# Kernel tuning notes

Measured on AMD Instinct MI355X. Metric: run time of the kernel, lower is better.

Reference implementation:

```python
import jax, jax.numpy as jnp
import numpy as np

N_NODES = 30000
N_EDGES = 480000
IN_SIZE = 256
EDGE_FEAT = 32
N_TOWERS = 4
DELTA = 2.5


def setup_inputs():
    key = jax.random.key(0)
    ks = jax.random.split(key, 8)
    T, d = N_TOWERS, IN_SIZE // N_TOWERS
    m_in = 2 * d + EDGE_FEAT                 # M: Linear(2*tower_in+edge_feat -> tower_in)
    u_in = (4 * 3 + 1) * d                   # U: Linear((n_agg*n_scaler+1)*tower_in -> tower_out)
    return {
        "n_feat": jax.random.normal(ks[0], (N_NODES, IN_SIZE), jnp.float32),
        "e_feat": jax.random.normal(ks[1], (N_EDGES, EDGE_FEAT), jnp.float32),
        "src": jax.random.randint(ks[2], (N_EDGES,), 0, N_NODES),
        "dst": jax.random.randint(ks[3], (N_EDGES,), 0, N_NODES),
        "M_w": jax.random.normal(ks[4], (T, d, m_in), jnp.float32) * (1.0 / np.sqrt(m_in)),
        "M_b": jnp.zeros((T, d), jnp.float32),
        "U_w": jax.random.normal(ks[5], (T, d, u_in), jnp.float32) * (1.0 / np.sqrt(u_in)),
        "U_b": jnp.zeros((T, d), jnp.float32),
        "bn_gamma": jnp.ones((T, d), jnp.float32),
        "bn_beta": jnp.zeros((T, d), jnp.float32),
        "mix_w": jax.random.normal(ks[6], (IN_SIZE, IN_SIZE), jnp.float32) * (1.0 / np.sqrt(IN_SIZE)),
        "mix_b": jnp.zeros((IN_SIZE,), jnp.float32),
    }


def reference(n_feat, e_feat, src, dst, M_w, M_b, U_w, U_b, bn_gamma, bn_beta, mix_w, mix_b):
    N, F = n_feat.shape
    T, d, _ = M_w.shape
    E = src.shape[0]
    h = n_feat.reshape(N, T, d)                                   # towers split the feature dim
    ef = jnp.broadcast_to(e_feat[:, None, :], (E, T, e_feat.shape[1]))
    f = jnp.concatenate([h[src], h[dst], ef], axis=-1)            # [E,T,2d+ef]
    msg = jnp.einsum('eti,toi->eto', f, M_w) + M_b                # per-edge message, [E,T,d]

    deg = jax.ops.segment_sum(jnp.ones((E,), msg.dtype), dst, num_segments=N)  # in-degree
    degc = jnp.maximum(deg, 1.0)[:, None, None]
    s = jax.ops.segment_sum(msg, dst, num_segments=N)
    ssq = jax.ops.segment_sum(msg * msg, dst, num_segments=N)
    mean = s / degc
    var = jax.nn.relu(ssq / degc - mean * mean)                   # DGL aggregate_var
    std = jnp.sqrt(var + 1e-30)                                   # DGL aggregate_std
    has = (deg > 0.0)[:, None, None]
    mx = jnp.where(has, jax.ops.segment_max(msg, dst, num_segments=N), 0.0)
    mn = jnp.where(has, jax.ops.segment_min(msg, dst, num_segments=N), 0.0)
    agg = jnp.concatenate([mean, mx, mn, std], axis=-1)           # [N,T,4d]

    logd = jnp.log(deg + 1.0)
    amp = (logd / DELTA)[:, None, None]                            # amplification scaler
    att = jnp.where(deg > 0.0, DELTA / jnp.maximum(logd, 1e-12), 0.0)[:, None, None]  # attenuation
    hsc = jnp.concatenate([agg, agg * amp, agg * att], axis=-1)   # [N,T,12d]

    u_in = jnp.concatenate([h, hsc], axis=-1)                     # [N,T,13d]
    u = jnp.einsum('nti,toi->nto', u_in, U_w) + U_b               # [N,T,d]
    mu = jnp.mean(u, axis=0)
    v = jnp.mean((u - mu) ** 2, axis=0)
    u = (u - mu) / jnp.sqrt(v + 1e-5) * bn_gamma + bn_beta        # BatchNorm1d (training mode)

    h_cat = u.reshape(N, F)
    mixed = h_cat @ mix_w.T + mix_b
    mixed = jnp.where(mixed > 0, mixed, 0.01 * mixed)             # LeakyReLU mixing layer
    out = mixed + n_feat                                          # residual (in_size==out_size)
    return jax.nn.relu(out)                                       # last == 0 -> ReLU
```

## Files before the change

### kernel.cpp

```cpp
#include <hip/hip_runtime.h>
#include <math.h>

constexpr float DELTA_ = 2.5f;
#define BN_BLOCKS 512

typedef __attribute__((ext_vector_type(8))) short bf16x8;
typedef __attribute__((ext_vector_type(4))) float f32x4;
typedef __attribute__((ext_vector_type(2))) _Float16 half2_t;

#if defined(__has_builtin)
#if __has_builtin(__builtin_amdgcn_fdot2)
#define DOT2(a,b,c) __builtin_amdgcn_fdot2((a),(b),(c),false)
#endif
#endif
#ifndef DOT2
#define DOT2(a,b,c) fmaf((float)(a).x,(float)(b).x, fmaf((float)(a).y,(float)(b).y,(c)))
#endif

__device__ inline ushort bf16h(float x){
  union { float f; unsigned u; } v; v.f = x;
  unsigned r = v.u + 0x7fffu + ((v.u >> 16) & 1u);
  return (ushort)(r >> 16);
}
__device__ inline float bf16f(ushort h){
  union { unsigned u; float f; } v; v.u = ((unsigned)h) << 16;
  return v.f;
}

__global__ __launch_bounds__(256) void k_tU(const float* __restrict__ Uw, ushort* __restrict__ Wpk2){
  int i = blockIdx.x*256 + threadIdx.x;
  if (i >= 4*192*320) return;
  int k   = i % 320;
  int col = (i/320) % 192;
  int t   = i/(320*192);
  int path = col >> 6, o = col & 63;
  float v = 0.f;
  int src = -1;
  if (k < 64){ if (path == 0) src = k; }
  else        src = k + path*256;
  if (src >= 0) v = Uw[((size_t)(t*64 + o))*832 + src];
  Wpk2[i] = bf16h(v);
}

__global__ __launch_bounds__(256) void k_tMm(const float* __restrict__ mixw, ushort* __restrict__ Wm2){
  int i = blockIdx.x*256 + threadIdx.x;
  if (i >= 256*256) return;
  Wm2[i] = bf16h(mixw[i]);
}

__global__ __launch_bounds__(256) void k_tE(const float* __restrict__ Mw, _Float16* __restrict__ Mwefh){
  int i = blockIdx.x*256 + threadIdx.x;
  if (i >= 256*32) return;
  int k = i & 31, c = i >> 5;
  Mwefh[i] = (_Float16)Mw[(size_t)c*160 + 128 + k];
}

__global__ __launch_bounds__(256) void k_xh(const float* __restrict__ nf, ushort* __restrict__ X2, int N){
  for (long i = blockIdx.x*256 + threadIdx.x; i < (long)N*256; i += (long)gridDim.x*256){
    int n = (int)(i >> 8), c = (int)(i & 255);
    int t = c >> 6, d = c & 63;
    int j = d >> 3, pos = d & 7;
    float v = nf[i];
    ushort hi = bf16h(v);
    size_t base = (((size_t)n*4 + t)*40 + j)*16;
    X2[base + pos]     = hi;
    X2[base + 8 + pos] = bf16h(v - bf16f(hi));
  }
}

__global__ __launch_bounds__(256) void k_hist(const int* __restrict__ dstv, int* __restrict__ cnt, int E){
  int e = blockIdx.x*256 + threadIdx.x;
  if (e < E) atomicAdd(&cnt[dstv[e]], 1);
}

__global__ __launch_bounds__(256) void k_scan1(const int* __restrict__ cnt, int* __restrict__ offs,
                                               int* __restrict__ bsum, int N){
  __shared__ int lds[256];
  int i = threadIdx.x;
  int g = blockIdx.x*256 + i;
  int v = (g < N) ? cnt[g] : 0;
  int acc = v;
  lds[i] = acc; __syncthreads();
  for (int s = 1; s < 256; s <<= 1){
    int t = (i >= s) ? lds[i - s] : 0;
    __syncthreads();
    acc += t; lds[i] = acc;
    __syncthreads();
  }
  if (g < N) offs[g] = acc - v;
  if (i == 255) bsum[blockIdx.x] = acc;
}

__global__ __launch_bounds__(256) void k_scan2(int* __restrict__ bsum, int NB){
  __shared__ int lds[256];
  int i = threadIdx.x;
  int v = (i < NB) ? bsum[i] : 0;
  int acc = v;
  lds[i] = acc; __syncthreads();
  for (int s = 1; s < 256; s <<= 1){
    int t = (i >= s) ? lds[i - s] : 0;
    __syncthreads();
    acc += t; lds[i] = acc;
    __syncthreads();
  }
  if (i < NB) bsum[i] = acc - v;
}

__global__ __launch_bounds__(256) void k_scan3(int* __restrict__ offs, const int* __restrict__ bsum, int N, int E){
  int g = blockIdx.x*256 + threadIdx.x;
  if (g < N) offs[g] += bsum[blockIdx.x];
  if (g == 0) offs[N] = E;
}

__global__ __launch_bounds__(256) void k_fill(const int* __restrict__ dstv, const int* __restrict__ offs,
                                              int* __restrict__ cur, int* __restrict__ elist, int E){
  int e = blockIdx.x*256 + threadIdx.x;
  if (e < E){
    int d = dstv[e];
    elist[offs[d] + atomicAdd(&cur[d], 1)] = e;
  }
}

__global__ __launch_bounds__(256) void k_perm(const int* __restrict__ elist, const int* __restrict__ srcv,
                                              const float* __restrict__ efeat,
                                              int* __restrict__ esrc, _Float16* __restrict__ efh, int E){
  int g = blockIdx.x*256 + threadIdx.x;
  int pos = g >> 3;
  int q   = g & 7;
  if (pos >= E) return;
  int e = elist[pos];
  if (q == 0) esrc[pos] = srcv[e];
  float4 v = *(const float4*)(efeat + (size_t)e*32 + q*4);
  union { ushort4 u; _Float16 h[4]; } cv;
  cv.h[0] = (_Float16)v.x; cv.h[1] = (_Float16)v.y;
  cv.h[2] = (_Float16)v.z; cv.h[3] = (_Float16)v.w;
  *(ushort4*)(efh + (size_t)pos*32 + q*4) = cv.u;
}

__global__ __launch_bounds__(256) void k_ab(const float* __restrict__ nf, const float* __restrict__ Mw,
                                            const float* __restrict__ Mb,
                                            _Float16* __restrict__ A_h, float* __restrict__ B, int N){
  int c = threadIdx.x;
  int t = __builtin_amdgcn_readfirstlane(threadIdx.x >> 6);
  float ws[64], wd[64];
  const float* row = Mw + (size_t)c*160;
#pragma unroll
  for (int k = 0; k < 64; k += 4){
    float4 a = *(const float4*)(row + k);
    float4 b = *(const float4*)(row + 64 + k);
    ws[k]=a.x; ws[k+1]=a.y; ws[k+2]=a.z; ws[k+3]=a.w;
    wd[k]=b.x; wd[k+1]=b.y; wd[k+2]=b.z; wd[k+3]=b.w;
  }
  float bias = Mb[c];
  for (int n = blockIdx.x; n < N; n += gridDim.x){
    const float* h = nf + (size_t)n*256 + t*64;
    float sa = 0.f, sb = 0.f;
#pragma unroll
    for (int k = 0; k < 64; k += 4){
      float4 h4 = *(const float4*)(h + k);
      sa = fmaf(ws[k], h4.x, sa);  sb = fmaf(wd[k], h4.x, sb);
      sa = fmaf(ws[k+1], h4.y, sa); sb = fmaf(wd[k+1], h4.y, sb);
      sa = fmaf(ws[k+2], h4.z, sa); sb = fmaf(wd[k+2], h4.z, sb);
      sa = fmaf(ws[k+3], h4.w, sa); sb = fmaf(wd[k+3], h4.w, sb);
    }
    A_h[(size_t)n*256 + c] = (_Float16)sa;
    B[(size_t)n*256 + c] = sb + bias;
  }
}

__global__ __launch_bounds__(256) void k_agg(const int* __restrict__ offs, const int* __restrict__ esrc,
                                             const _Float16* __restrict__ efh,
                                             const _Float16* __restrict__ A_h, const float* __restrict__ B,
                                             const _Float16* __restrict__ Mwefh,
                                             ushort* __restrict__ X2, float* __restrict__ sc, int N){
  int c = threadIdx.x;
  union Wu { int4 i[4]; half2_t h[16]; } wr;
  {
    const int4* wp = (const int4*)(Mwefh + (size_t)c*32);
    wr.i[0] = wp[0]; wr.i[1] = wp[1]; wr.i[2] = wp[2]; wr.i[3] = wp[3];
  }

  int n = blockIdx.x;
  if (n >= N) return;
  int o0 = __builtin_amdgcn_readfirstlane(offs[n]);
  int o1 = __builtin_amdgcn_readfirstlane(offs[n+1]);
  int cnt = o1 - o0;
  float b0 = B[(size_t)n*256 + c];
  float s = 0.f, ss = 0.f, mx = -__builtin_huge_valf(), mn = __builtin_huge_valf();

  union Eu { int4 i[4]; half2_t h[16]; };

  int i = 0;
  for (; i + 4 <= cnt; i += 4){
    int p = o0 + i;
    int s0 = __builtin_amdgcn_readfirstlane(esrc[p+0]);
    int s1 = __builtin_amdgcn_readfirstlane(esrc[p+1]);
    int s2 = __builtin_amdgcn_readfirstlane(esrc[p+2]);
    int s3 = __builtin_amdgcn_readfirstlane(esrc[p+3]);
    Eu e0, e1, e2, e3;
    {
      const int4* p0 = (const int4*)(efh + (size_t)(p+0)*32);
      const int4* p1 = (const int4*)(efh + (size_t)(p+1)*32);
      const int4* p2 = (const int4*)(efh + (size_t)(p+2)*32);
      const int4* p3 = (const int4*)(efh + (size_t)(p+3)*32);
#pragma unroll
      for (int q = 0; q < 4; ++q){ e0.i[q]=p0[q]; e1.i[q]=p1[q]; e2.i[q]=p2[q]; e3.i[q]=p3[q]; }
    }
    float a0 = (float)A_h[(size_t)s0*256 + c];
    float a1 = (float)A_h[(size_t)s1*256 + c];
    float a2 = (float)A_h[(size_t)s2*256 + c];
    float a3 = (float)A_h[(size_t)s3*256 + c];
    float m0 = b0 + a0;
    float m1 = b0 + a1;
    float m2 = b0 + a2;
    float m3 = b0 + a3;
#pragma unroll
    for (int q = 0; q < 16; ++q){
      m0 = DOT2(e0.h[q], wr.h[q], m0);
      m1 = DOT2(e1.h[q], wr.h[q], m1);
      m2 = DOT2(e2.h[q], wr.h[q], m2);
      m3 = DOT2(e3.h[q], wr.h[q], m3);
    }
    s += m0; s += m1; s += m2; s += m3;
    ss = fmaf(m0, m0, ss); ss = fmaf(m1, m1, ss);
    ss = fmaf(m2, m2, ss); ss = fmaf(m3, m3, ss);
    mx = fmaxf(mx, fmaxf(fmaxf(m0, m1), fmaxf(m2, m3)));
    mn = fminf(mn, fminf(fminf(m0, m1), fminf(m2, m3)));
  }
  for (; i < cnt; ++i){
    int p = o0 + i;
    int sidx = __builtin_amdgcn_readfirstlane(esrc[p]);
    Eu e0;
    {
      const int4* p0 = (const int4*)(efh + (size_t)p*32);
#pragma unroll
      for (int q = 0; q < 4; ++q) e0.i[q] = p0[q];
    }
    float m = b0 + (float)A_h[(size_t)sidx*256 + c];
#pragma unroll
    for (int q = 0; q < 16; ++q) m = DOT2(e0.h[q], wr.h[q], m);
    s += m;
    ss = fmaf(m, m, ss);
    mx = fmaxf(mx, m);
    mn = fminf(mn, m);
  }

  float deg  = (float)cnt;
  float degc = fmaxf(deg, 1.f);
  float inv  = 1.f / degc;
  float mean = s * inv;
  float var  = fmaxf(ss * inv - mean*mean, 0.f);
  float sd   = sqrtf(var + 1e-30f);
  if (cnt == 0){ mx = 0.f; mn = 0.f; }

  int t = c >> 6, d = c & 63;
#define PUTX(SLOT, VAL) { int kk = 64 + (SLOT)*64 + d; int jj = kk >> 3, pp = kk & 7;      \
    size_t base = (((size_t)n*4 + t)*40 + jj)*16;                                          \
    ushort hi = bf16h(VAL);                                                                \
    X2[base + pp] = hi; X2[base + 8 + pp] = bf16h((VAL) - bf16f(hi)); }
  PUTX(0, mean) PUTX(1, mx) PUTX(2, mn) PUTX(3, sd)
#undef PUTX
  if (c == 0){
    float logd = logf(deg + 1.f);
    sc[(size_t)n*2]     = logd * (1.f / DELTA_);
    sc[(size_t)n*2 + 1] = (cnt > 0) ? (DELTA_ / fmaxf(logd, 1e-12f)) : 0.f;
  }
}

__global__ __launch_bounds__(256) void k_u(const ushort* __restrict__ X2, const ushort* __restrict__ Wpk2,
                                           const float* __restrict__ sc, const float* __restrict__ Ub,
                                           float* __restrict__ uout, int Nn){
  __shared__ float su[64][68];
  int tid = threadIdx.x;
  int t   = blockIdx.y;
  int nbase = blockIdx.x*64;
  int lane = tid & 63, wv = tid >> 6;
  int li = lane & 15, kc = lane >> 4;
  int cbase = wv*48;

  f32x4 acc[4][3];
#pragma unroll
  for (int ri = 0; ri < 4; ++ri)
#pragma unroll
    for (int ci = 0; ci < 3; ++ci) acc[ri][ci] = (f32x4)0.f;

  const ushort* wb = Wpk2 + (size_t)t*192*320;

#pragma unroll 2
  for (int kt = 0; kt < 10; ++kt){
    bf16x8 ah[4], al[4], bh[3];
#pragma unroll
    for (int ri = 0; ri < 4; ++ri){
      int row = nbase + ri*16 + li;
      if (row >= Nn) row = Nn - 1;
      const ushort* ap = X2 + (((size_t)row*4 + t)*40 + kt*4 + kc)*16;
      ah[ri] = *(const bf16x8*)(ap);
      al[ri] = *(const bf16x8*)(ap + 8);
    }
#pragma unroll
    for (int ci = 0; ci < 3; ++ci){
      int col = cbase + ci*16 + li;
      bh[ci] = *(const bf16x8*)(wb + (size_t)col*320 + kt*32 + kc*8);
    }
#pragma unroll
    for (int ci = 0; ci < 3; ++ci)
#pragma unroll
      for (int ri = 0; ri < 4; ++ri){
        acc[ri][ci] = __builtin_amdgcn_mfma_f32_16x16x32_bf16(ah[ri], bh[ci], acc[ri][ci], 0, 0, 0);
        acc[ri][ci] = __builtin_amdgcn_mfma_f32_16x16x32_bf16(al[ri], bh[ci], acc[ri][ci], 0, 0, 0);
      }
  }

#define Y1_STORE(CI, OB) { _Pragma("unroll") for (int ri = 0; ri < 4; ++ri)               \
    { _Pragma("unroll") for (int r = 0; r < 4; ++r)                                        \
      su[ri*16 + kc*4 + r][(OB) + li] = acc[ri][CI][r]; } }
#define Y_ADD(CI, OB, SCOFF) { _Pragma("unroll") for (int ri = 0; ri < 4; ++ri)           \
    { _Pragma("unroll") for (int r = 0; r < 4; ++r){                                       \
      int node = ri*16 + kc*4 + r;                                                        \
      int gn = nbase + node; int gnc = (gn < Nn) ? gn : (Nn - 1);                          \
      float scl = sc[(size_t)gnc*2 + (SCOFF)];                                            \
      su[node][(OB) + li] += scl * acc[ri][CI][r]; } } }

  if (wv == 0){ Y1_STORE(0, 0)  Y1_STORE(1, 16) Y1_STORE(2, 32) }
  else if (wv == 1){ Y1_STORE(0, 48) }
  __syncthreads();
  if (wv == 1){ Y_ADD(1, 0, 0)  Y_ADD(2, 16, 0) }
  else if (wv == 2){ Y_ADD(0, 32, 0) Y_ADD(1, 48, 0) }
  __syncthreads();
  if (wv == 2){ Y_ADD(2, 0, 1) }
  else if (wv == 3){ Y_ADD(0, 16, 1) Y_ADD(1, 32, 1) Y_ADD(2, 48, 1) }
  __syncthreads();
#undef Y1_STORE
#undef Y_ADD

  for (int idx = tid; idx < 64*16; idx += 256){
    int n = idx >> 4, o4 = (idx & 15)*4;
    int gn = nbase + n;
    if (gn < Nn){
      float4 v = *(float4*)(&su[n][o4]);
      const float* ubp = Ub + t*64 + o4;
      v.x += ubp[0]; v.y += ubp[1]; v.z += ubp[2]; v.w += ubp[3];
      *(float4*)(&uout[(size_t)gn*256 + t*64 + o4]) = v;
    }
  }
}

__global__ __launch_bounds__(256) void k_bnstat(const float* __restrict__ u, float* __restrict__ part, int N){
  int c = threadIdx.x;
  int b = blockIdx.x;
  float s = 0.f, ss = 0.f;
  for (int n = b; n < N; n += gridDim.x){
    float v = u[(size_t)n*256 + c];
    s += v;
    ss = fmaf(v, v, ss);
  }
  part[(size_t)b*512 + c]       = s;
  part[(size_t)b*512 + 256 + c] = ss;
}

__global__ __launch_bounds__(256) void k_bnfin(const float* __restrict__ part, const float* __restrict__ gam,
                                               const float* __restrict__ bet, float* __restrict__ bnsc, int N){
  int c = threadIdx.x;
  float s = 0.f, ss = 0.f;
  for (int b = 0; b < BN_BLOCKS; ++b){
    s  += part[(size_t)b*512 + c];
    ss += part[(size_t)b*512 + 256 + c];
  }
  float invN = 1.f / (float)N;
  float mu  = s * invN;
  float ex2 = ss * invN;
  float var = fmaxf(ex2 - mu*mu, 0.f);
  float inv = 1.f / sqrtf(var + 1e-5f);
  float scale = gam[c] * inv;
  bnsc[c]       = scale;
  bnsc[256 + c] = bet[c] - mu*scale;
}

__global__ __launch_bounds__(256) void k_xm(const float* __restrict__ u, const float* __restrict__ bnsc,
                                            ushort* __restrict__ X2m, int N){
  for (long i = blockIdx.x*256 + threadIdx.x; i < (long)N*256; i += (long)gridDim.x*256){
    int n = (int)(i >> 8), c = (int)(i & 255);
    float v = fmaf(u[i], bnsc[c], bnsc[256 + c]);
    int j = c >> 3, pos = c & 7;
    size_t base = ((size_t)n*32 + j)*16;
    ushort hi = bf16h(v);
    X2m[base + pos]     = hi;
    X2m[base + 8 + pos] = bf16h(v - bf16f(hi));
  }
}

__global__ __launch_bounds__(256) void k_mix(const ushort* __restrict__ X2m, const ushort* __restrict__ Wm2,
                                             const float* __restrict__ mixb, const float* __restrict__ nf,
                                             float* __restrict__ outp, int Nn){
  int tid = threadIdx.x;
  int nbase = blockIdx.x*64;
  int lane = tid & 63, wv = tid >> 6;
  int li = lane & 15, kc = lane >> 4;

  f32x4 acc[4][4];
#pragma unroll
  for (int ri = 0; ri < 4; ++ri)
#pragma unroll
    for (int ci = 0; ci < 4; ++ci) acc[ri][ci] = (f32x4)0.f;

#pragma unroll 2
  for (int kt = 0; kt < 8; ++kt){
    bf16x8 ah[4], al[4], bh[4];
#pragma unroll
    for (int ri = 0; ri < 4; ++ri){
      int row = nbase + ri*16 + li;
      if (row >= Nn) row = Nn - 1;
      const ushort* ap = X2m + (((size_t)row*32 + kt*4 + kc))*16;
      ah[ri] = *(const bf16x8*)(ap);
      al[ri] = *(const bf16x8*)(ap + 8);
    }
#pragma unroll
    for (int ci = 0; ci < 4; ++ci){
      int col = wv*64 + ci*16 + li;
      bh[ci] = *(const bf16x8*)(Wm2 + (size_t)col*256 + kt*32 + kc*8);
    }
#pragma unroll
    for (int ci = 0; ci < 4; ++ci)
#pragma unroll
      for (int ri = 0; ri < 4; ++ri){
        acc[ri][ci] = __builtin_amdgcn_mfma_f32_16x16x32_bf16(ah[ri], bh[ci], acc[ri][ci], 0, 0, 0);
        acc[ri][ci] = __builtin_amdgcn_mfma_f32_16x16x32_bf16(al[ri], bh[ci], acc[ri][ci], 0, 0, 0);
      }
  }

#pragma unroll
  for (int ri = 0; ri < 4; ++ri){
#pragma unroll
    for (int r = 0; r < 4; ++r){
      int node = ri*16 + kc*4 + r;
      int gn = nbase + node;
      if (gn < Nn){
#pragma unroll
        for (int ci = 0; ci < 4; ++ci){
          int col = wv*64 + ci*16 + li;
          float m = acc[ri][ci][r] + mixb[col];
          m = (m > 0.f) ? m : 0.01f*m;
          float o = m + nf[(size_t)gn*256 + col];
          outp[(size_t)gn*256 + col] = fmaxf(o, 0.f);
        }
      }
    }
  }
}

extern "C" void kernel_launch(void* const* d_in, const int* in_sizes, int n_in,
                              void* d_out, int out_size, void* d_ws, size_t ws_size,
                              hipStream_t stream){
  const float* nf   = (const float*)d_in[0];
  const float* ef   = (const float*)d_in[1];
  const int*   srcv = (const int*)  d_in[2];
  const int*   dstv = (const int*)  d_in[3];
  const float* Mw   = (const float*)d_in[4];
  const float* Mb   = (const float*)d_in[5];
  const float* Uw   = (const float*)d_in[6];
  const float* Ub   = (const float*)d_in[7];
  const float* gam  = (const float*)d_in[8];
  const float* bet  = (const float*)d_in[9];
  const float* mixw = (const float*)d_in[10];
  const float* mixb = (const float*)d_in[11];
  int N = in_sizes[0] / 256;
  int E = in_sizes[2];
  float* out = (float*)d_out;

  char* wp = (char*)d_ws;
  auto alloc = [&](size_t bytes){
    char* p = wp;
    wp += (bytes + 1023) & ~(size_t)1023;
    return (void*)p;
  };
  int*      cnt   = (int*)     alloc((size_t)N*4);
  int*      offs  = (int*)     alloc((size_t)(N+1)*4);
  int*      cur   = (int*)     alloc((size_t)N*4);
  int*      bsum  = (int*)     alloc(256*4);
  int*      elist = (int*)     alloc((size_t)E*4);
  int*      esrc  = (int*)     alloc((size_t)E*4);
  size_t ealias   = (size_t)E*32*2;
  size_t malias   = (size_t)N*512*2;
  char*     shbuf = (char*)    alloc(ealias > malias ? ealias : malias);
  _Float16* efh   = (_Float16*)shbuf;
  ushort*   X2m   = (ushort*)  shbuf;
  _Float16* A_h   = (_Float16*)alloc((size_t)N*256*2);
  float*    B     = (float*)   alloc((size_t)N*256*4);
  float*    sc    = (float*)   alloc((size_t)N*2*4);
  float*    part  = (float*)   alloc((size_t)BN_BLOCKS*512*4);
  float*    bnsc  = (float*)   alloc(512*4);
  ushort*   X2    = (ushort*)  alloc((size_t)N*4*40*16*2);
  ushort*   Wpk2  = (ushort*)  alloc((size_t)4*192*320*2);
  ushort*   Wm2   = (ushort*)  alloc((size_t)256*256*2);
  _Float16* Mwefh = (_Float16*)alloc((size_t)256*32*2);

  hipMemsetAsync(cnt,  0, (size_t)N*4,  stream);
  hipMemsetAsync(cur,  0, (size_t)N*4,  stream);

  k_tU  <<<(4*192*320 + 255)/256, 256, 0, stream>>>(Uw, Wpk2);
  k_tMm <<<(256*256 + 255)/256, 256, 0, stream>>>(mixw, Wm2);
  k_tE  <<<(256*32 + 255)/256, 256, 0, stream>>>(Mw, Mwefh);
  k_hist<<<(E + 255)/256, 256, 0, stream>>>(dstv, cnt, E);
  k_ab  <<<2048, 256, 0, stream>>>(nf, Mw, Mb, A_h, B, N);
  k_xh  <<<2048, 256, 0, stream>>>(nf, X2, N);

  int NB = (N + 255)/256;
  k_scan1<<<NB, 256, 0, stream>>>(cnt, offs, bsum, N);
  k_scan2<<<1, 256, 0, stream>>>(bsum, NB);
  k_scan3<<<NB, 256, 0, stream>>>(offs, bsum, N, E);
  k_fill <<<(E + 255)/256, 256, 0, stream>>>(dstv, offs, cur, elist, E);
  k_perm <<<(E*8 + 255)/256, 256, 0, stream>>>(elist, srcv, ef, esrc, efh, E);

  k_agg<<<N, 256, 0, stream>>>(offs, esrc, efh, A_h, B, Mwefh, X2, sc, N);

  dim3 ugrid((N + 63)/64, 4);
  k_u<<<ugrid, 256, 0, stream>>>(X2, Wpk2, sc, Ub, out, N);

  k_bnstat<<<BN_BLOCKS, 256, 0, stream>>>(out, part, N);
  k_bnfin <<<1, 256, 0, stream>>>(part, gam, bet, bnsc, N);
  k_xm   <<<2048, 256, 0, stream>>>(out, bnsc, X2m, N);
  k_mix  <<<(N + 63)/64, 256, 0, stream>>>(X2m, Wm2, mixb, nf, out, N);
}
```

Baseline: 493.8 us.

## Compute edge-feature projection with MFMA over edge windows, 8 nodes per block

The aggregation kernel now handles 8 destination nodes per block and walks their contiguous edge range in windows of 64 edges. For each window it computes the edge-feature projection with f16 MFMA instructions into shared memory, replacing per-thread fdot2 loops. It also factors the per-node bias out of the message sums, adding it back algebraically at finalize time. The node-boundary loop is serial and adds syncthreads and a 66KB shared tile, which may reduce occupancy, and the factored variance is numerically less stable.

```diff
diff --git a/kernel.cpp b/kernel.cpp
--- a/kernel.cpp
+++ b/kernel.cpp
@@ -3,19 +3,11 @@
 
 constexpr float DELTA_ = 2.5f;
 #define BN_BLOCKS 512
+#define NPB 8
 
 typedef __attribute__((ext_vector_type(8))) short bf16x8;
+typedef __attribute__((ext_vector_type(8))) _Float16 f16x8;
 typedef __attribute__((ext_vector_type(4))) float f32x4;
-typedef __attribute__((ext_vector_type(2))) _Float16 half2_t;
-
-#if defined(__has_builtin)
-#if __has_builtin(__builtin_amdgcn_fdot2)
-#define DOT2(a,b,c) __builtin_amdgcn_fdot2((a),(b),(c),false)
-#endif
-#endif
-#ifndef DOT2
-#define DOT2(a,b,c) fmaf((float)(a).x,(float)(b).x, fmaf((float)(a).y,(float)(b).y,(c)))
-#endif
 
 __device__ inline ushort bf16h(float x){
   union { float f; unsigned u; } v; v.f = x;
@@ -48,11 +40,15 @@
   Wm2[i] = bf16h(mixw[i]);
 }
 
-__global__ __launch_bounds__(256) void k_tE(const float* __restrict__ Mw, _Float16* __restrict__ Mwefh){
+__global__ __launch_bounds__(256) void k_tE2(const float* __restrict__ Mw, _Float16* __restrict__ Wefp){
   int i = blockIdx.x*256 + threadIdx.x;
-  if (i >= 256*32) return;
-  int k = i & 31, c = i >> 5;
-  Mwefh[i] = (_Float16)Mw[(size_t)c*160 + 128 + k];
+  if (i >= 16*64*8) return;
+  int j    = i & 7;
+  int lane = (i >> 3) & 63;
+  int cb   = i >> 9;
+  int ch = cb*16 + (lane & 15);
+  int k  = ((lane >> 4) & 3)*8 + j;
+  Wefp[i] = (_Float16)Mw[(size_t)ch*160 + 128 + k];
 }
 
 __global__ __launch_bounds__(256) void k_xh(const float* __restrict__ nf, ushort* __restrict__ X2, int N){
@@ -171,100 +167,115 @@
 __global__ __launch_bounds__(256) void k_agg(const int* __restrict__ offs, const int* __restrict__ esrc,
                                              const _Float16* __restrict__ efh,
                                              const _Float16* __restrict__ A_h, const float* __restrict__ B,
-                                             const _Float16* __restrict__ Mwefh,
-                                             ushort* __restrict__ X2, float* __restrict__ sc, int N){
-  int c = threadIdx.x;
-  union Wu { int4 i[4]; half2_t h[16]; } wr;
-  {
-    const int4* wp = (const int4*)(Mwefh + (size_t)c*32);
-    wr.i[0] = wp[0]; wr.i[1] = wp[1]; wr.i[2] = wp[2]; wr.i[3] = wp[3];
-  }
-
-  int n = blockIdx.x;
-  if (n >= N) return;
-  int o0 = __builtin_amdgcn_readfirstlane(offs[n]);
-  int o1 = __builtin_amdgcn_readfirstlane(offs[n+1]);
-  int cnt = o1 - o0;
-  float b0 = B[(size_t)n*256 + c];
-  float s = 0.f, ss = 0.f, mx = -__builtin_huge_valf(), mn = __builtin_huge_valf();
-
-  union Eu { int4 i[4]; half2_t h[16]; };
-
-  int i = 0;
-  for (; i + 4 <= cnt; i += 4){
-    int p = o0 + i;
-    int s0 = __builtin_amdgcn_readfirstlane(esrc[p+0]);
-    int s1 = __builtin_amdgcn_readfirstlane(esrc[p+1]);
-    int s2 = __builtin_amdgcn_readfirstlane(esrc[p+2]);
-    int s3 = __builtin_amdgcn_readfirstlane(esrc[p+3]);
-    Eu e0, e1, e2, e3;
-    {
-      const int4* p0 = (const int4*)(efh + (size_t)(p+0)*32);
-      const int4* p1 = (const int4*)(efh + (size_t)(p+1)*32);
-      const int4* p2 = (const int4*)(efh + (size_t)(p+2)*32);
-      const int4* p3 = (const int4*)(efh + (size_t)(p+3)*32);
-#pragma unroll
-      for (int q = 0; q < 4; ++q){ e0.i[q]=p0[q]; e1.i[q]=p1[q]; e2.i[q]=p2[q]; e3.i[q]=p3[q]; }
-    }
-    float a0 = (float)A_h[(size_t)s0*256 + c];
-    float a1 = (float)A_h[(size_t)s1*256 + c];
-    float a2 = (float)A_h[(size_t)s2*256 + c];
-    float a3 = (float)A_h[(size_t)s3*256 + c];
-    float m0 = b0 + a0;
-    float m1 = b0 + a1;
-    float m2 = b0 + a2;
-    float m3 = b0 + a3;
-#pragma unroll
-    for (int q = 0; q < 16; ++q){
-      m0 = DOT2(e0.h[q], wr.h[q], m0);
-      m1 = DOT2(e1.h[q], wr.h[q], m1);
-      m2 = DOT2(e2.h[q], wr.h[q], m2);
-      m3 = DOT2(e3.h[q], wr.h[q], m3);
-    }
-    s += m0; s += m1; s += m2; s += m3;
-    ss = fmaf(m0, m0, ss); ss = fmaf(m1, m1, ss);
-    ss = fmaf(m2, m2, ss); ss = fmaf(m3, m3, ss);
-    mx = fmaxf(mx, fmaxf(fmaxf(m0, m1), fmaxf(m2, m3)));
-    mn = fminf(mn, fminf(fminf(m0, m1), fminf(m2, m3)));
-  }
-  for (; i < cnt; ++i){
-    int p = o0 + i;
-    int sidx = __builtin_amdgcn_readfirstlane(esrc[p]);
-    Eu e0;
-    {
-      const int4* p0 = (const int4*)(efh + (size_t)p*32);
-#pragma unroll
-      for (int q = 0; q < 4; ++q) e0.i[q] = p0[q];
-    }
-    float m = b0 + (float)A_h[(size_t)sidx*256 + c];
-#pragma unroll
-    for (int q = 0; q < 16; ++q) m = DOT2(e0.h[q], wr.h[q], m);
-    s += m;
-    ss = fmaf(m, m, ss);
-    mx = fmaxf(mx, m);
-    mn = fminf(mn, m);
-  }
-
-  float deg  = (float)cnt;
-  float degc = fmaxf(deg, 1.f);
-  float inv  = 1.f / degc;
-  float mean = s * inv;
-  float var  = fmaxf(ss * inv - mean*mean, 0.f);
-  float sd   = sqrtf(var + 1e-30f);
-  if (cnt == 0){ mx = 0.f; mn = 0.f; }
-
-  int t = c >> 6, d = c & 63;
-#define PUTX(SLOT, VAL) { int kk = 64 + (SLOT)*64 + d; int jj = kk >> 3, pp = kk & 7;      \
-    size_t base = (((size_t)n*4 + t)*40 + jj)*16;                                          \
-    ushort hi = bf16h(VAL);                                                                \
-    X2[base + pp] = hi; X2[base + 8 + pp] = bf16h((VAL) - bf16f(hi)); }
-  PUTX(0, mean) PUTX(1, mx) PUTX(2, mn) PUTX(3, sd)
-#undef PUTX
-  if (c == 0){
-    float logd = logf(deg + 1.f);
-    sc[(size_t)n*2]     = logd * (1.f / DELTA_);
-    sc[(size_t)n*2 + 1] = (cnt > 0) ? (DELTA_ / fmaxf(logd, 1e-12f)) : 0.f;
-  }
+                                             const _Float16* __restrict__ Wefp,
+                                             ushort* __restrict__ X2, float* __restrict__ sc, int N, int E){
+  __shared__ float eps[64][260];
+  int tid = threadIdx.x;
+  int lane = tid & 63, wv = tid >> 6;
+  int li = lane & 15, kq = lane >> 4;
+  int c = tid;
+  int tw = c >> 6, d = c & 63;
+
+  int n0 = blockIdx.x * NPB;
+  if (n0 >= N) return;
+  int n1 = n0 + NPB; if (n1 > N) n1 = N;
+  int oS = offs[n0], oE = offs[n1];
+
+  f16x8 bf[4];
+#pragma unroll
+  for (int cbl = 0; cbl < 4; ++cbl)
+    bf[cbl] = *(const f16x8*)(Wefp + ((size_t)(wv*4 + cbl)*64 + lane)*8);
+
+  int cur = n0;
+  int curstart = oS;
+  int nextoff = offs[n0 + 1];
+  float s = 0.f, ss = 0.f;
+  float mx = -__builtin_huge_valf(), mn = __builtin_huge_valf();
+
+#define FINALIZE(CNT)                                                             \
+  {                                                                                \
+    float b = B[(size_t)cur*256 + c];                                              \
+    float deg = (float)(CNT);                                                      \
+    float degc = fmaxf(deg, 1.f);                                                  \
+    float inv = 1.f / degc;                                                        \
+    float S  = fmaf(deg, b, s);                                                    \
+    float SS = fmaf(deg, b*b, fmaf(2.f*b, s, ss));                                 \
+    float mean = S * inv;                                                          \
+    float var  = fmaxf(SS * inv - mean*mean, 0.f);                                 \
+    float sd   = sqrtf(var + 1e-30f);                                              \
+    float MX = ((CNT) > 0) ? (b + mx) : 0.f;                                       \
+    float MN = ((CNT) > 0) ? (b + mn) : 0.f;                                       \
+    size_t xb = (((size_t)cur*4 + tw)*40)*16;                                      \
+    { int kk = 64 + d;       ushort h2 = bf16h(mean);                              \
+      X2[xb + (kk>>3)*16 + (kk&7)] = h2;                                           \
+      X2[xb + (kk>>3)*16 + 8 + (kk&7)] = bf16h(mean - bf16f(h2)); }                \
+    { int kk = 128 + d;      ushort h2 = bf16h(MX);                                \
+      X2[xb + (kk>>3)*16 + (kk&7)] = h2;                                           \
+      X2[xb + (kk>>3)*16 + 8 + (kk&7)] = bf16h(MX - bf16f(h2)); }                  \
+    { int kk = 192 + d;      ushort h2 = bf16h(MN);                                \
+      X2[xb + (kk>>3)*16 + (kk&7)] = h2;                                           \
+      X2[xb + (kk>>3)*16 + 8 + (kk&7)] = bf16h(MN - bf16f(h2)); }                  \
+    { int kk = 256 + d;      ushort h2 = bf16h(sd);                                \
+      X2[xb + (kk>>3)*16 + (kk&7)] = h2;                                           \
+      X2[xb + (kk>>3)*16 + 8 + (kk&7)] = bf16h(sd - bf16f(h2)); }                  \
+    if (tid == 0){                                                                 \
+      float logd = logf(deg + 1.f);                                                \
+      sc[(size_t)cur*2]     = logd * (1.f / DELTA_);                               \
+      sc[(size_t)cur*2 + 1] = ((CNT) > 0) ? (DELTA_ / fmaxf(logd, 1e-12f)) : 0.f;  \
+    }                                                                              \
+  }
+
+  for (int w0 = oS; w0 < oE; w0 += 64){
+    __syncthreads();
+#pragma unroll
+    for (int ch = 0; ch < 4; ++ch){
+      int pos = w0 + ch*16 + li;
+      if (pos > E - 1) pos = E - 1;
+      f16x8 af = *(const f16x8*)(efh + (size_t)pos*32 + kq*8);
+      f32x4 ep0 = __builtin_amdgcn_mfma_f32_16x16x32_f16(af, bf[0], (f32x4)0.f, 0, 0, 0);
+      f32x4 ep1 = __builtin_amdgcn_mfma_f32_16x16x32_f16(af, bf[1], (f32x4)0.f, 0, 0, 0);
+      f32x4 ep2 = __builtin_amdgcn_mfma_f32_16x16x32_f16(af, bf[2], (f32x4)0.f, 0, 0, 0);
+      f32x4 ep3 = __builtin_amdgcn_mfma_f32_16x16x32_f16(af, bf[3], (f32x4)0.f, 0, 0, 0);
+#pragma unroll
+      for (int r = 0; r < 4; ++r){
+        int row = ch*16 + kq*4 + r;
+        eps[row][wv*64 +  0 + li] = ep0[r];
+        eps[row][wv*64 + 16 + li] = ep1[r];
+        eps[row][wv*64 + 32 + li] = ep2[r];
+        eps[row][wv*64 + 48 + li] = ep3[r];
+      }
+    }
+    __syncthreads();
+
+    int wend = w0 + 64; if (wend > oE) wend = oE;
+    for (int idx = w0; idx < wend; ++idx){
+      while (idx == nextoff){
+        FINALIZE(nextoff - curstart)
+        curstart = nextoff;
+        ++cur;
+        nextoff = offs[cur + 1];
+        s = 0.f; ss = 0.f;
+        mx = -__builtin_huge_valf(); mn = __builtin_huge_valf();
+      }
+      int src = __builtin_amdgcn_readfirstlane(esrc[idx]);
+      float a = (float)A_h[(size_t)src*256 + c];
+      float m = eps[idx - w0][c] + a;
+      s += m;
+      ss = fmaf(m, m, ss);
+      mx = fmaxf(mx, m);
+      mn = fminf(mn, m);
+    }
+  }
+
+  while (cur < n1){
+    FINALIZE(nextoff - curstart)
+    curstart = nextoff;
+    ++cur;
+    if (cur < n1) nextoff = offs[cur + 1];
+    s = 0.f; ss = 0.f;
+    mx = -__builtin_huge_valf(); mn = __builtin_huge_valf();
+  }
+#undef FINALIZE
 }
 
 __global__ __launch_bounds__(256) void k_u(const ushort* __restrict__ X2, const ushort* __restrict__ Wpk2,
@@ -492,14 +503,14 @@
   ushort*   X2    = (ushort*)  alloc((size_t)N*4*40*16*2);
   ushort*   Wpk2  = (ushort*)  alloc((size_t)4*192*320*2);
   ushort*   Wm2   = (ushort*)  alloc((size_t)256*256*2);
-  _Float16* Mwefh = (_Float16*)alloc((size_t)256*32*2);
+  _Float16* Wefp  = (_Float16*)alloc((size_t)16*64*8*2);
 
   hipMemsetAsync(cnt,  0, (size_t)N*4,  stream);
   hipMemsetAsync(cur,  0, (size_t)N*4,  stream);
 
   k_tU  <<<(4*192*320 + 255)/256, 256, 0, stream>>>(Uw, Wpk2);
   k_tMm <<<(256*256 + 255)/256, 256, 0, stream>>>(mixw, Wm2);
-  k_tE  <<<(256*32 + 255)/256, 256, 0, stream>>>(Mw, Mwefh);
+  k_tE2 <<<(16*64*8 + 255)/256, 256, 0, stream>>>(Mw, Wefp);
   k_hist<<<(E + 255)/256, 256, 0, stream>>>(dstv, cnt, E);
   k_ab  <<<2048, 256, 0, stream>>>(nf, Mw, Mb, A_h, B, N);
   k_xh  <<<2048, 256, 0, stream>>>(nf, X2, N);
@@ -511,7 +522,7 @@
   k_fill <<<(E + 255)/256, 256, 0, stream>>>(dstv, offs, cur, elist, E);
   k_perm <<<(E*8 + 255)/256, 256, 0, stream>>>(elist, srcv, ef, esrc, efh, E);
 
-  k_agg<<<N, 256, 0, stream>>>(offs, esrc, efh, A_h, B, Mwefh, X2, sc, N);
+  k_agg<<<(N + NPB - 1)/NPB, 256, 0, stream>>>(offs, esrc, efh, A_h, B, Wefp, X2, sc, N, E);
 
   dim3 ugrid((N + 63)/64, 4);
   k_u<<<ugrid, 256, 0, stream>>>(X2, Wpk2, sc, Ub, out, N);
```

Result: slower. 760.0 us (+53.9%).
